# Kernel optimization log

Hardware: AMD Instinct MI355X
Metric: run time of the kernel (lower is better)

## Reference

```python
import jax, jax.numpy as jnp
import numpy as np

N = 102400          # total nodes (256 graphs x 400 nodes)
E = 3276800         # edges (avg degree 32)
B = 256             # num graphs
NODE_DIM, MRI_DIM, COG_DIM, CLIN_DIM, GEN_DIM, NUM_CLASSES = 128, 256, 64, 32, 512, 3
EPS = 1e-5

def _lin(k, i, o):
    kw, kb = jax.random.split(k)
    s = 1.0 / np.sqrt(i)
    return (jax.random.uniform(kw, (i, o), jnp.float32, -s, s),
            jax.random.uniform(kb, (o,), jnp.float32, -s, s))

def setup_inputs() -> dict:
    key = jax.random.key(0)
    ks = jax.random.split(key, 20)
    inp = {}
    inp['x'] = jax.random.normal(ks[0], (N, NODE_DIM), jnp.float32)
    inp['edge_index'] = jax.random.randint(ks[1], (2, E), 0, N)
    inp['batch'] = jnp.repeat(jnp.arange(B, dtype=jnp.int32), N // B)
    inp['mri'] = jax.random.normal(ks[2], (B, MRI_DIM), jnp.float32)
    inp['cog'] = jax.random.normal(ks[3], (B, COG_DIM), jnp.float32)
    inp['clin'] = jax.random.normal(ks[4], (B, CLIN_DIM), jnp.float32)
    inp['gen'] = jax.random.normal(ks[5], (B, GEN_DIM), jnp.float32)
    inp['W1'], inp['b1'] = _lin(ks[6], NODE_DIM, 64)
    inp['W2'], inp['b2'] = _lin(ks[7], 64, 32)
    inp['W3'], inp['b3'] = _lin(ks[8], 32, 16)
    inp['bn1_g'] = jnp.ones((64,), jnp.float32); inp['bn1_b'] = jnp.zeros((64,), jnp.float32)
    inp['bn2_g'] = jnp.ones((32,), jnp.float32); inp['bn2_b'] = jnp.zeros((32,), jnp.float32)
    inp['mriW'], inp['mrib'] = _lin(ks[9], MRI_DIM, 16)
    inp['cogW'], inp['cogb'] = _lin(ks[10], COG_DIM, 16)
    inp['clinW'], inp['clinb'] = _lin(ks[11], CLIN_DIM, 16)
    inp['genW'], inp['genb'] = _lin(ks[12], GEN_DIM, 16)
    inp['c1W'], inp['c1b'] = _lin(ks[13], 96, 64)  # 32 (pooled) + 64 (multimodal)
    inp['cbn1_g'] = jnp.ones((64,), jnp.float32); inp['cbn1_b'] = jnp.zeros((64,), jnp.float32)
    inp['c2W'], inp['c2b'] = _lin(ks[14], 64, 32)
    inp['cbn2_g'] = jnp.ones((32,), jnp.float32); inp['cbn2_b'] = jnp.zeros((32,), jnp.float32)
    inp['c3W'], inp['c3b'] = _lin(ks[15], 32, NUM_CLASSES)
    return inp

def _bn(h, g, b):
    # BatchNorm1d in training mode: biased batch stats
    m = h.mean(0)
    v = jnp.mean((h - m) ** 2, 0)
    return (h - m) * jax.lax.rsqrt(v + EPS) * g + b

def _gcn(h, W, bias, s, d, norm):
    # GCNConv: linear -> symmetric-normalized scatter-add aggregation (self-loops in s/d)
    h = h @ W
    agg = jnp.zeros_like(h).at[d].add(h[s] * norm[:, None])
    return agg + bias

def reference(x, edge_index, batch, mri, cog, clin, gen,
              W1, b1, W2, b2, W3, b3, bn1_g, bn1_b, bn2_g, bn2_b,
              mriW, mrib, cogW, cogb, clinW, clinb, genW, genb,
              c1W, c1b, cbn1_g, cbn1_b, c2W, c2b, cbn2_g, cbn2_b, c3W, c3b):
    n = x.shape[0]
    loop = jnp.arange(n)
    s = jnp.concatenate([edge_index[0], loop])
    d = jnp.concatenate([edge_index[1], loop])
    deg = jnp.zeros((n,), x.dtype).at[d].add(1.0)
    dinv = jax.lax.rsqrt(deg)  # deg >= 1 due to self-loops
    norm = dinv[s] * dinv[d]

    x1 = jax.nn.relu(_bn(_gcn(x, W1, b1, s, d, norm), bn1_g, bn1_b))
    x2 = jax.nn.relu(_bn(_gcn(x1, W2, b2, s, d, norm), bn2_g, bn2_b))
    gf = jax.nn.relu(_gcn(x2, W3, b3, s, d, norm))  # [N,16]

    cnt = jax.ops.segment_sum(jnp.ones((n,), x.dtype), batch, num_segments=B)
    g_mean = jax.ops.segment_sum(gf, batch, num_segments=B) / cnt[:, None]
    g_max = jax.ops.segment_max(gf, batch, num_segments=B)
    g_emb = jnp.concatenate([g_mean, g_max], axis=1)  # [B,32]

    mm = jnp.concatenate([
        jax.nn.relu(mri @ mriW + mrib),
        jax.nn.relu(cog @ cogW + cogb),
        jax.nn.relu(clin @ clinW + clinb),
        jax.nn.relu(gen @ genW + genb)], axis=1)  # [B,64]

    h = jnp.concatenate([g_emb, mm], axis=1)  # [B,96]
    h = jax.nn.relu(_bn(h @ c1W + c1b, cbn1_g, cbn1_b))  # dropout = identity (eval)
    h = jax.nn.relu(_bn(h @ c2W + c2b, cbn2_g, cbn2_b))
    out = h @ c3W + c3b
    return jax.nn.log_softmax(out, axis=1)
```

## Files before the change

kernel.cpp:

```cpp
#include <hip/hip_runtime.h>
#include <hip/hip_bf16.h>

#define TPB 256
#define BSHIFT 9
#define BNODES 512
#define CH 4096

typedef unsigned long long u64;
typedef __attribute__((ext_vector_type(8))) short short8;
typedef __attribute__((ext_vector_type(4))) float f32x4;

__device__ inline unsigned short f2bf(float f) {
    unsigned u = __float_as_uint(f);
    return (unsigned short)((u + 0x7FFF + ((u >> 16) & 1)) >> 16);
}
__device__ inline float bf2f(short s) {
    return __uint_as_float(((unsigned)(unsigned short)s) << 16);
}


__global__ void k_bhist(const int* __restrict__ dstp, int* __restrict__ bcnt, int E, int nbuk) {
    __shared__ int h[256];
    int tid = threadIdx.x;
    h[tid] = 0;
    __syncthreads();
    int e0 = blockIdx.x * CH;
    int e1 = min(e0 + CH, E);
    for (int e = e0 + tid; e < e1; e += TPB) atomicAdd(&h[dstp[e] >> BSHIFT], 1);
    __syncthreads();
    if (tid < nbuk && h[tid]) atomicAdd(&bcnt[tid], h[tid]);
}

__global__ void k_bscan(const int* __restrict__ bcnt, int* __restrict__ bbase,
                        int* __restrict__ gcur, int nbuk, int E) {
    __shared__ int s[256];
    int tid = threadIdx.x;
    int v = (tid < nbuk) ? bcnt[tid] : 0;
    s[tid] = v;
    __syncthreads();
    for (int o = 1; o < 256; o <<= 1) {
        int t = (tid >= o) ? s[tid - o] : 0;
        __syncthreads();
        s[tid] += t;
        __syncthreads();
    }
    if (tid < nbuk) { int e = s[tid] - v; bbase[tid] = e; gcur[tid] = e; }
    if (tid == 0) bbase[nbuk] = E;
}

__global__ void k_partition(const int* __restrict__ ei, int* __restrict__ gcur,
                            u64* __restrict__ part, int E, int nbuk) {
    __shared__ int h[256], baseg[256], scn[256], cur[256];
    __shared__ u64 stage[CH];
    int tid = threadIdx.x;
    h[tid] = 0;
    __syncthreads();
    int e0 = blockIdx.x * CH;
    int ecnt = min(CH, E - e0);
    const int* srcp = ei;
    const int* dstp = ei + E;
    for (int i = tid; i < ecnt; i += TPB) atomicAdd(&h[dstp[e0 + i] >> BSHIFT], 1);
    __syncthreads();
    int v = h[tid];
    if (tid < nbuk && v) baseg[tid] = atomicAdd(&gcur[tid], v);
    scn[tid] = v;
    __syncthreads();
    for (int o = 1; o < 256; o <<= 1) {
        int t = (tid >= o) ? scn[tid - o] : 0;
        __syncthreads();
        scn[tid] += t;
        __syncthreads();
    }
    int excl = scn[tid] - v;
    __syncthreads();
    scn[tid] = excl; cur[tid] = excl;
    __syncthreads();
    for (int i = tid; i < ecnt; i += TPB) {
        int s = srcp[e0 + i], d = dstp[e0 + i];
        int bk = d >> BSHIFT;
        int p = atomicAdd(&cur[bk], 1);
        stage[p] = ((u64)(unsigned)d << 32) | (unsigned)s;
    }
    __syncthreads();
    for (int i = tid; i < ecnt; i += TPB) {
        u64 vv = stage[i];
        int bk = (int)(vv >> 32) >> BSHIFT;
        part[baseg[bk] + (i - scn[bk])] = vv;
    }
}

__global__ void k_bucket_csr(const u64* __restrict__ part, const int* __restrict__ bbase,
                             float* __restrict__ dinv, int* __restrict__ offsets,
                             int* __restrict__ csr, int N, int nbuk) {
    __shared__ int cnt[BNODES];
    __shared__ int ps[256];
    __shared__ int off_s[BNODES];
    int b = blockIdx.x, tid = threadIdx.x;
    int n0 = b << BSHIFT;
    int nn = min(BNODES, N - n0);
    int j0 = bbase[b], j1 = bbase[b + 1];
    for (int i = tid; i < BNODES; i += TPB) cnt[i] = 0;
    __syncthreads();
    for (int j = j0 + tid; j < j1; j += TPB) {
        int dst = (int)(part[j] >> 32);
        atomicAdd(&cnt[dst - n0], 1);
    }
    __syncthreads();
    int a0 = cnt[2 * tid], a1 = cnt[2 * tid + 1];
    ps[tid] = a0 + a1;
    __syncthreads();
    for (int o = 1; o < 256; o <<= 1) {
        int t = (tid >= o) ? ps[tid - o] : 0;
        __syncthreads();
        ps[tid] += t;
        __syncthreads();
    }
    int excl = ps[tid] - (a0 + a1);
    off_s[2 * tid] = excl;
    off_s[2 * tid + 1] = excl + a0;
    __syncthreads();
    for (int i = tid; i < nn; i += TPB) {
        dinv[n0 + i] = rsqrtf((float)(cnt[i] + 1));
        offsets[n0 + i] = j0 + off_s[i];
    }
    if (b == nbuk - 1 && tid == 0) offsets[N] = j1;
    __syncthreads();
    for (int i = tid; i < BNODES; i += TPB) cnt[i] = j0 + off_s[i];
    __syncthreads();
    for (int j = j0 + tid; j < j1; j += TPB) {
        u64 vv = part[j];
        int dst = (int)(vv >> 32);
        int src = (int)(vv & 0xffffffffu);
        int pos = atomicAdd(&cnt[dst - n0], 1);
        csr[pos] = src;
    }
}


template<int K, bool BN, bool BF16IN>
__global__ void k_packA(const void* __restrict__ inv, const float* __restrict__ scale,
                        const float* __restrict__ shift, unsigned short* __restrict__ out) {
    constexpr int KB = K / 32;
    int g = blockIdx.x * TPB + threadIdx.x;
    int lane = g & 63, tile = g >> 6;
    int rowblk = tile / KB, kblk = tile - rowblk * KB;
    int row = rowblk * 16 + (lane & 15);
    int k0 = kblk * 32 + (lane >> 4) * 8;
    float vs[8];
    if (BF16IN) {
        const __hip_bfloat16* in = (const __hip_bfloat16*)inv;
        short8 sv = *reinterpret_cast<const short8*>(in + (size_t)row * K + k0);
        #pragma unroll
        for (int u = 0; u < 8; ++u) vs[u] = bf2f(sv[u]);
    } else {
        const float* in = (const float*)inv;
        const float4* p = reinterpret_cast<const float4*>(in + (size_t)row * K + k0);
        float4 v0 = p[0], v1 = p[1];
        vs[0] = v0.x; vs[1] = v0.y; vs[2] = v0.z; vs[3] = v0.w;
        vs[4] = v1.x; vs[5] = v1.y; vs[6] = v1.z; vs[7] = v1.w;
    }
    short8 rr;
    #pragma unroll
    for (int u = 0; u < 8; ++u) {
        float v = vs[u];
        if (BN) v = fmaxf(v * scale[k0 + u] + shift[k0 + u], 0.f);
        rr[u] = (short)f2bf(v);
    }
    *reinterpret_cast<short8*>(out + (size_t)g * 8) = rr;
}

__global__ void k_packW(const float* __restrict__ W1, const float* __restrict__ W2,
                        const float* __restrict__ W3, unsigned short* __restrict__ out) {
    int b = blockIdx.x, lane = threadIdx.x;
    const float* W; int KB, C; size_t off; int idx;
    if (b < 16)      { W = W1; KB = 4; C = 64; off = 0;     idx = b; }
    else if (b < 20) { W = W2; KB = 2; C = 32; off = 8192;  idx = b - 16; }
    else             { W = W3; KB = 1; C = 16; off = 10240; idx = b - 20; }
    int nblk = idx / KB, kblk = idx - nblk * KB;
    int col = nblk * 16 + (lane & 15);
    int k0 = kblk * 32 + (lane >> 4) * 8;
    short8 rr;
    #pragma unroll
    for (int j = 0; j < 8; ++j) rr[j] = (short)f2bf(W[(size_t)(k0 + j) * C + col]);
    *reinterpret_cast<short8*>(out + off + ((size_t)idx * 64 + lane) * 8) = rr;
}

template<int K, int C, int SW>
__global__ void k_mfma_gemm(const unsigned short* __restrict__ A,
                            const unsigned short* __restrict__ Wp,
                            const float* __restrict__ dinv,
                            __hip_bfloat16* __restrict__ hh, size_t slice) {
    constexpr int KB = K / 32, NB = C / 16;
    int lane = threadIdx.x & 63, w = threadIdx.x >> 6;
    int rowblk = blockIdx.x * 4 + w;
    const short8* Af = reinterpret_cast<const short8*>(A);
    const short8* Bf = reinterpret_cast<const short8*>(Wp);
    short8 b[NB][KB];
    #pragma unroll
    for (int nb = 0; nb < NB; ++nb)
        #pragma unroll
        for (int kb = 0; kb < KB; ++kb)
            b[nb][kb] = Bf[(nb * KB + kb) * 64 + lane];
    f32x4 z = {0.f, 0.f, 0.f, 0.f};
    f32x4 acc[NB];
    #pragma unroll
    for (int nb = 0; nb < NB; ++nb) acc[nb] = z;
    #pragma unroll
    for (int kb = 0; kb < KB; ++kb) {
        short8 a = Af[((size_t)rowblk * KB + kb) * 64 + lane];
        #pragma unroll
        for (int nb = 0; nb < NB; ++nb)
            acc[nb] = __builtin_amdgcn_mfma_f32_16x16x32_bf16(a, b[nb][kb], acc[nb], 0, 0, 0);
    }
    int colb = lane & 15;
    int node0 = rowblk * 16 + (lane >> 4) * 4;
    float dv[4];
    #pragma unroll
    for (int j = 0; j < 4; ++j) dv[j] = dinv[node0 + j];
    #pragma unroll
    for (int nb = 0; nb < NB; ++nb) {
        int c = nb * 16 + colb;
        size_t base = (size_t)(c / SW) * slice + (c % SW);
        #pragma unroll
        for (int j = 0; j < 4; ++j)
            hh[base + (size_t)(node0 + j) * SW] = __float2bfloat16(acc[nb][j] * dv[j]);
    }
}

template<int CT, bool RELU, bool STATS>
__global__ void k_gather_row32(const __hip_bfloat16* __restrict__ hhp,
                               const int* __restrict__ offs, const int* __restrict__ csr,
                               const float* __restrict__ dinv, const float* __restrict__ bias,
                               __hip_bfloat16* __restrict__ outp, float* __restrict__ pstat,
                               int n) {
    __shared__ float lred[16 * 528];
    __shared__ float sred[2 * 544];
    int tid = threadIdx.x;
    int g = tid >> 4, l = tid & 15;
    int node = blockIdx.x * 16 + g;
    int j0 = offs[node], j1 = offs[node + 1];
    float facc[32];
    #pragma unroll
    for (int u = 0; u < 32; ++u) facc[u] = 0.f;
    if (l == 15) {
        const short8* sr = reinterpret_cast<const short8*>(hhp + (size_t)node * 32);
        short8 r0 = sr[0], r1 = sr[1], r2 = sr[2], r3 = sr[3];
        #pragma unroll
        for (int u = 0; u < 8; ++u) {
            facc[u] += bf2f(r0[u]);      facc[8 + u]  += bf2f(r1[u]);
            facc[16 + u] += bf2f(r2[u]); facc[24 + u] += bf2f(r3[u]);
        }
    }
    int j = j0 + l;
    for (; j + 16 < j1; j += 32) {
        int s0 = __builtin_nontemporal_load(&csr[j]);
        int s1 = __builtin_nontemporal_load(&csr[j + 16]);
        const short8* ra = reinterpret_cast<const short8*>(hhp + (size_t)s0 * 32);
        const short8* rb = reinterpret_cast<const short8*>(hhp + (size_t)s1 * 32);
        short8 a0 = ra[0], a1 = ra[1], a2 = ra[2], a3 = ra[3];
        short8 b0 = rb[0], b1 = rb[1], b2 = rb[2], b3 = rb[3];
        #pragma unroll
        for (int u = 0; u < 8; ++u) {
            facc[u]      += bf2f(a0[u]) + bf2f(b0[u]);
            facc[8 + u]  += bf2f(a1[u]) + bf2f(b1[u]);
            facc[16 + u] += bf2f(a2[u]) + bf2f(b2[u]);
            facc[24 + u] += bf2f(a3[u]) + bf2f(b3[u]);
        }
    }
    if (j < j1) {
        int s = __builtin_nontemporal_load(&csr[j]);
        const short8* rr = reinterpret_cast<const short8*>(hhp + (size_t)s * 32);
        short8 r0 = rr[0], r1 = rr[1], r2 = rr[2], r3 = rr[3];
        #pragma unroll
        for (int u = 0; u < 8; ++u) {
            facc[u] += bf2f(r0[u]);      facc[8 + u]  += bf2f(r1[u]);
            facc[16 + u] += bf2f(r2[u]); facc[24 + u] += bf2f(r3[u]);
        }
    }
    int wbase = g * 528 + l * 33;
    #pragma unroll
    for (int u = 0; u < 32; ++u) lred[wbase + u] = facc[u];
    __syncthreads();
    int rbase = g * 528 + l;
    float alo = 0.f, ahi = 0.f;
    #pragma unroll
    for (int k = 0; k < 16; ++k) {
        alo += lred[rbase + k * 33];
        ahi += lred[rbase + k * 33 + 16];
    }
    float dv = dinv[node];
    float vlo = dv * alo + bias[l];
    float vhi = dv * ahi + bias[l + 16];
    if (RELU) { vlo = fmaxf(vlo, 0.f); vhi = fmaxf(vhi, 0.f); }
    outp[(size_t)node * CT + l]      = __float2bfloat16(vlo);
    outp[(size_t)node * CT + l + 16] = __float2bfloat16(vhi);
    if (STATS) {
        sred[l * 17 + g]          = vlo;
        sred[(l + 16) * 17 + g]   = vhi;
        sred[544 + l * 17 + g]        = vlo * vlo;
        sred[544 + (l + 16) * 17 + g] = vhi * vhi;
        __syncthreads();
        if (tid < 64) {
            int which = tid >> 5, c = tid & 31;
            const float* base = sred + which * 544 + c * 17;
            float a = 0.f;
            #pragma unroll
            for (int k = 0; k < 16; ++k) a += base[k];
            pstat[(size_t)blockIdx.x * 64 + which * 32 + c] = a;
        }
    }
}

template<int CT, bool RELU>
__global__ void k_gather_row(const __hip_bfloat16* __restrict__ hhp,
                             const int* __restrict__ offs, const int* __restrict__ csr,
                             const float* __restrict__ dinv, const float* __restrict__ bias,
                             __hip_bfloat16* __restrict__ outp, int n) {
    __shared__ float lred[16 * 272];
    int tid = threadIdx.x;
    int g = tid >> 4, l = tid & 15;
    int node = blockIdx.x * 16 + g;
    int j0 = offs[node], j1 = offs[node + 1];
    float facc[16];
    #pragma unroll
    for (int u = 0; u < 16; ++u) facc[u] = 0.f;
    if (l == 15) {
        const short8* sr = reinterpret_cast<const short8*>(hhp + (size_t)node * 16);
        short8 r0 = sr[0], r1 = sr[1];
        #pragma unroll
        for (int u = 0; u < 8; ++u) { facc[u] += bf2f(r0[u]); facc[8 + u] += bf2f(r1[u]); }
    }
    int j = j0 + l;
    for (; j + 16 < j1; j += 32) {
        int s0 = __builtin_nontemporal_load(&csr[j]);
        int s1 = __builtin_nontemporal_load(&csr[j + 16]);
        const short8* ra = reinterpret_cast<const short8*>(hhp + (size_t)s0 * 16);
        const short8* rb = reinterpret_cast<const short8*>(hhp + (size_t)s1 * 16);
        short8 a0 = ra[0], a1 = ra[1], b0 = rb[0], b1 = rb[1];
        #pragma unroll
        for (int u = 0; u < 8; ++u) {
            facc[u]     += bf2f(a0[u]) + bf2f(b0[u]);
            facc[8 + u] += bf2f(a1[u]) + bf2f(b1[u]);
        }
    }
    if (j < j1) {
        int s = __builtin_nontemporal_load(&csr[j]);
        const short8* rr = reinterpret_cast<const short8*>(hhp + (size_t)s * 16);
        short8 r0 = rr[0], r1 = rr[1];
        #pragma unroll
        for (int u = 0; u < 8; ++u) { facc[u] += bf2f(r0[u]); facc[8 + u] += bf2f(r1[u]); }
    }
    int wbase = g * 272 + l * 17;
    #pragma unroll
    for (int u = 0; u < 16; ++u) lred[wbase + u] = facc[u];
    __syncthreads();
    int rbase = g * 272 + l;
    float acc = 0.f;
    #pragma unroll
    for (int k = 0; k < 16; ++k) acc += lred[rbase + k * 17];
    float v = dinv[node] * acc + bias[l];
    if (RELU) v = fmaxf(v, 0.f);
    outp[(size_t)node * CT + l] = __float2bfloat16(v);
}

__global__ void k_bnred(const float* __restrict__ pstat, float* __restrict__ bred, int G) {
    __shared__ float ss[256];
    int tid = threadIdx.x;
    int p = blockIdx.x >> 6, c = blockIdx.x & 63;
    int rows_per = (G + 63) >> 6;
    int r0 = c * rows_per, r1 = min(r0 + rows_per, G);
    const float* base = pstat + (size_t)p * G * 64;
    float acc = 0.f;
    for (int i = r0 * 64 + tid; i < r1 * 64; i += 256) acc += base[i];
    ss[tid] = acc;
    __syncthreads();
    #pragma unroll
    for (int o = 128; o >= 64; o >>= 1) {
        if (tid < o) ss[tid] += ss[tid + o];
        __syncthreads();
    }
    if (tid < 64) bred[(size_t)blockIdx.x * 64 + tid] = ss[tid];
}

__global__ void k_bnstat2(const float* __restrict__ bred, const float* __restrict__ g,
                          const float* __restrict__ b, float* __restrict__ scale,
                          float* __restrict__ shift, float invN) {
    __shared__ float ss[256];
    int tid = threadIdx.x, p = blockIdx.x;
    const float* base = bred + (size_t)p * 64 * 64;
    float acc = 0.f;
    for (int i = tid; i < 64 * 64; i += 256) acc += base[i];
    ss[tid] = acc;
    __syncthreads();
    #pragma unroll
    for (int o = 128; o >= 64; o >>= 1) {
        if (tid < o) ss[tid] += ss[tid + o];
        __syncthreads();
    }
    if (tid < 32) {
        int ch = p * 32 + tid;
        float m = ss[tid] * invN;
        float var = ss[32 + tid] * invN - m * m;
        float sc = g[ch] * rsqrtf(var + 1e-5f);
        scale[ch] = sc;
        shift[ch] = b[ch] - m * sc;
    }
}

__global__ void k_graphhead(const __hip_bfloat16* __restrict__ gf, int nper,
                            const float* __restrict__ mri, const float* __restrict__ cog,
                            const float* __restrict__ clin, const float* __restrict__ gen,
                            const float* __restrict__ mriW, const float* __restrict__ mrib,
                            const float* __restrict__ cogW, const float* __restrict__ cogb,
                            const float* __restrict__ clinW, const float* __restrict__ clinb,
                            const float* __restrict__ genW, const float* __restrict__ genb,
                            const float* __restrict__ c1W, const float* __restrict__ c1b,
                            float* __restrict__ t1) {
    __shared__ float ssum[TPB], smax[TPB];
    __shared__ float hb[96];
    int b = blockIdx.x, tid = threadIdx.x;
    {
        int c = tid & 15, r0 = tid >> 4;
        const __hip_bfloat16* base = gf + (size_t)b * nper * 16;
        float s = 0.f, m = -1e30f;
        for (int r = r0; r < nper; r += 16) {
            float v = __bfloat162float(base[r * 16 + c]);
            s += v; m = fmaxf(m, v);
        }
        ssum[tid] = s; smax[tid] = m; __syncthreads();
        for (int off = 128; off >= 16; off >>= 1) {
            if (tid < off) { ssum[tid] += ssum[tid + off]; smax[tid] = fmaxf(smax[tid], smax[tid + off]); }
            __syncthreads();
        }
        if (tid < 16) { hb[tid] = ssum[tid] / (float)nper; hb[16 + tid] = smax[tid]; }
    }
    {
        int w = tid >> 6, lane = tid & 63;
        int c = lane & 15, part = lane >> 4;
        const float* in; const float* W; const float* bias; int K;
        if (w == 0)      { in = mri  + b * 256; W = mriW;  bias = mrib;  K = 256; }
        else if (w == 1) { in = cog  + b * 64;  W = cogW;  bias = cogb;  K = 64;  }
        else if (w == 2) { in = clin + b * 32;  W = clinW; bias = clinb; K = 32;  }
        else             { in = gen  + b * 512; W = genW;  bias = genb;  K = 512; }
        int kq = K >> 2, k0 = part * kq;
        float acc = 0.f;
        for (int k = k0; k < k0 + kq; k += 4) {
            float4 iv = *reinterpret_cast<const float4*>(in + k);
            acc += iv.x * W[k * 16 + c] + iv.y * W[(k + 1) * 16 + c]
                 + iv.z * W[(k + 2) * 16 + c] + iv.w * W[(k + 3) * 16 + c];
        }
        acc += __shfl_xor(acc, 16);
        acc += __shfl_xor(acc, 32);
        if (part == 0) hb[32 + w * 16 + c] = fmaxf(acc + bias[c], 0.f);
    }
    __syncthreads();
    if (tid < 64) {
        float acc = c1b[tid];
        #pragma unroll
        for (int k = 0; k < 96; ++k) acc += hb[k] * c1W[k * 64 + tid];
        t1[b * 64 + tid] = acc;
    }
}

__global__ __launch_bounds__(1024) void k_headtail(
        float* __restrict__ t1g,
        const float* __restrict__ cbn1_g, const float* __restrict__ cbn1_b,
        const float* __restrict__ c2W, const float* __restrict__ c2b,
        const float* __restrict__ cbn2_g, const float* __restrict__ cbn2_b,
        const float* __restrict__ c3W, const float* __restrict__ c3b,
        float* __restrict__ out) {
    __shared__ float red[1024];
    __shared__ float t2s[256 * 32];
    __shared__ float sc1[64], sh1[64], sc2[32], sh2[32];
    int tid = threadIdx.x;
    const float invB = 1.0f / 256.0f;

    float psum = 0.f, psq = 0.f;
    for (int i = tid; i < 16384; i += 1024) {
        float v = t1g[i]; psum += v; psq += v * v;
    }
    red[tid] = psum; __syncthreads();
    for (int o = 512; o >= 64; o >>= 1) { if (tid < o) red[tid] += red[tid + o]; __syncthreads(); }
    if (tid < 64) sc1[tid] = red[tid];
    __syncthreads();
    red[tid] = psq; __syncthreads();
    for (int o = 512; o >= 64; o >>= 1) { if (tid < o) red[tid] += red[tid + o]; __syncthreads(); }
    if (tid < 64) {
        float m = sc1[tid] * invB;
        float var = red[tid] * invB - m * m;
        float s = cbn1_g[tid] * rsqrtf(var + 1e-5f);
        sc1[tid] = s; sh1[tid] = cbn1_b[tid] - m * s;
    }
    __syncthreads();
    for (int i = tid; i < 16384; i += 1024) {
        int k = i & 63;
        t1g[i] = fmaxf(t1g[i] * sc1[k] + sh1[k], 0.f);
    }
    __syncthreads();
    int j2 = tid & 31, g2 = tid >> 5;
    float p2 = 0.f, q2 = 0.f;
    for (int b = g2 * 8; b < g2 * 8 + 8; ++b) {
        const float* tr = t1g + b * 64;
        float acc = c2b[j2];
        #pragma unroll
        for (int k = 0; k < 64; ++k) acc += tr[k] * c2W[k * 32 + j2];
        t2s[b * 32 + j2] = acc; p2 += acc; q2 += acc * acc;
    }
    red[tid] = p2; __syncthreads();
    for (int o = 512; o >= 32; o >>= 1) { if (tid < o) red[tid] += red[tid + o]; __syncthreads(); }
    if (tid < 32) sc2[tid] = red[tid];
    __syncthreads();
    red[tid] = q2; __syncthreads();
    for (int o = 512; o >= 32; o >>= 1) { if (tid < o) red[tid] += red[tid + o]; __syncthreads(); }
    if (tid < 32) {
        float m = sc2[tid] * invB;
        float var = red[tid] * invB - m * m;
        float s = cbn2_g[tid] * rsqrtf(var + 1e-5f);
        sc2[tid] = s; sh2[tid] = cbn2_b[tid] - m * s;
    }
    __syncthreads();
    if (tid < 256) {
        const float* tr = t2s + tid * 32;
        float o0 = c3b[0], o1 = c3b[1], o2 = c3b[2];
        #pragma unroll
        for (int k = 0; k < 32; ++k) {
            float v = fmaxf(tr[k] * sc2[k] + sh2[k], 0.f);
            o0 += v * c3W[k * 3 + 0];
            o1 += v * c3W[k * 3 + 1];
            o2 += v * c3W[k * 3 + 2];
        }
        float m = fmaxf(fmaxf(o0, o1), o2);
        float lse = m + logf(expf(o0 - m) + expf(o1 - m) + expf(o2 - m));
        out[tid * 3 + 0] = o0 - lse;
        out[tid * 3 + 1] = o1 - lse;
        out[tid * 3 + 2] = o2 - lse;
    }
}


extern "C" void kernel_launch(void* const* d_in, const int* in_sizes, int n_in,
                              void* d_out, int out_size, void* d_ws, size_t ws_size,
                              hipStream_t stream) {
    const float* x    = (const float*)d_in[0];
    const int*   ei   = (const int*)d_in[1];
    const float* mri  = (const float*)d_in[3];
    const float* cog  = (const float*)d_in[4];
    const float* clin = (const float*)d_in[5];
    const float* gen  = (const float*)d_in[6];
    const float* W1 = (const float*)d_in[7];  const float* b1 = (const float*)d_in[8];
    const float* W2 = (const float*)d_in[9];  const float* b2 = (const float*)d_in[10];
    const float* W3 = (const float*)d_in[11]; const float* b3 = (const float*)d_in[12];
    const float* bn1_g = (const float*)d_in[13]; const float* bn1_b = (const float*)d_in[14];
    const float* bn2_g = (const float*)d_in[15]; const float* bn2_b = (const float*)d_in[16];
    const float* mriW = (const float*)d_in[17]; const float* mrib = (const float*)d_in[18];
    const float* cogW = (const float*)d_in[19]; const float* cogb = (const float*)d_in[20];
    const float* clinW = (const float*)d_in[21]; const float* clinb = (const float*)d_in[22];
    const float* genW = (const float*)d_in[23]; const float* genb = (const float*)d_in[24];
    const float* c1W = (const float*)d_in[25]; const float* c1b = (const float*)d_in[26];
    const float* cbn1_g = (const float*)d_in[27]; const float* cbn1_b = (const float*)d_in[28];
    const float* c2W = (const float*)d_in[29]; const float* c2b = (const float*)d_in[30];
    const float* cbn2_g = (const float*)d_in[31]; const float* cbn2_b = (const float*)d_in[32];
    const float* c3W = (const float*)d_in[33]; const float* c3b = (const float*)d_in[34];
    float* out = (float*)d_out;

    const int N = in_sizes[0] / 128;
    const int E = in_sizes[1] / 2;
    const int B = in_sizes[6] / 512;
    const int nper = N / B;
    const int nbuk = (N + BNODES - 1) >> BSHIFT;
    const int npart = (E + CH - 1) / CH;
    const int rowblks = N / 16;
    const int G = N / 16;

    char* ws = (char*)d_ws;
    size_t off = 0;
    auto alloc = [&](size_t bytes) -> void* {
        void* p = ws + off;
        off += (bytes + 255) & ~(size_t)255;
        return p;
    };
    int*   bcnt    = (int*)alloc(256 * 4);
    int*   bbase   = (int*)alloc((size_t)(nbuk + 1) * 4);
    int*   gcur    = (int*)alloc((size_t)nbuk * 4);
    u64*   part    = (u64*)alloc((size_t)E * 8);
    __hip_bfloat16* agg = (__hip_bfloat16*)part;
    int*   offsets = (int*)alloc((size_t)(N + 1) * 4);
    int*   csr     = (int*)alloc((size_t)E * 4);
    float* dinv    = (float*)alloc((size_t)N * 4);
    __hip_bfloat16* hh = (__hip_bfloat16*)alloc((size_t)N * 64 * 2);
    unsigned short* xb = (unsigned short*)alloc((size_t)N * 128 * 2);
    unsigned short* Wpack = (unsigned short*)alloc(10752 * 2);
    float* pstat   = (float*)alloc((size_t)3 * G * 64 * 4);
    float* bred    = (float*)alloc((size_t)3 * 64 * 64 * 4);
    float* scale1  = (float*)alloc(64 * 4);
    float* shift1  = (float*)alloc(64 * 4);
    float* scale2  = (float*)alloc(32 * 4);
    float* shift2  = (float*)alloc(32 * 4);
    float* t1      = (float*)alloc((size_t)B * 64 * 4);
    (void)ws_size; (void)n_in; (void)out_size;

    hipMemsetAsync(bcnt, 0, 256 * 4, stream);

    k_bhist<<<npart, TPB, 0, stream>>>(ei + E, bcnt, E, nbuk);
    k_bscan<<<1, TPB, 0, stream>>>(bcnt, bbase, gcur, nbuk, E);
    k_partition<<<npart, TPB, 0, stream>>>(ei, gcur, part, E, nbuk);
    k_bucket_csr<<<nbuk, TPB, 0, stream>>>(part, bbase, dinv, offsets, csr, N, nbuk);
    k_packW<<<21, 64, 0, stream>>>(W1, W2, W3, Wpack);

    size_t slice32 = (size_t)N * 32;
    int gmm = rowblks / 4;

    k_packA<128, false, false><<<rowblks * 4 * 64 / TPB, TPB, 0, stream>>>(x, nullptr, nullptr, xb);
    k_mfma_gemm<128, 64, 32><<<gmm, TPB, 0, stream>>>(xb, Wpack, dinv, hh, slice32);
    for (int p = 0; p < 2; ++p)
        k_gather_row32<64, false, true><<<G, TPB, 0, stream>>>(
            hh + p * slice32, offsets, csr, dinv, b1 + p * 32,
            agg + p * 32, pstat + (size_t)p * G * 64, N);
    k_bnred<<<2 * 64, 256, 0, stream>>>(pstat, bred, G);
    k_bnstat2<<<2, 256, 0, stream>>>(bred, bn1_g, bn1_b, scale1, shift1, 1.0f / N);

    k_packA<64, true, true><<<rowblks * 2 * 64 / TPB, TPB, 0, stream>>>(agg, scale1, shift1, xb);
    k_mfma_gemm<64, 32, 32><<<gmm, TPB, 0, stream>>>(xb, Wpack + 8192, dinv, hh, slice32);
    k_gather_row32<32, false, true><<<G, TPB, 0, stream>>>(
        hh, offsets, csr, dinv, b2, agg, pstat + (size_t)2 * G * 64, N);
    k_bnred<<<64, 256, 0, stream>>>(pstat + (size_t)2 * G * 64, bred + 2 * 64 * 64, G);
    k_bnstat2<<<1, 256, 0, stream>>>(bred + 2 * 64 * 64, bn2_g, bn2_b, scale2, shift2, 1.0f / N);

    k_packA<32, true, true><<<rowblks * 1 * 64 / TPB, TPB, 0, stream>>>(agg, scale2, shift2, xb);
    k_mfma_gemm<32, 16, 16><<<gmm, TPB, 0, stream>>>(xb, Wpack + 10240, dinv, hh, (size_t)N * 16);
    k_gather_row<16, true><<<G, TPB, 0, stream>>>(hh, offsets, csr, dinv, b3, agg, N);

    k_graphhead<<<B, TPB, 0, stream>>>(agg, nper, mri, cog, clin, gen,
                                       mriW, mrib, cogW, cogb, clinW, clinb, genW, genb,
                                       c1W, c1b, t1);
    k_headtail<<<1, 1024, 0, stream>>>(t1, cbn1_g, cbn1_b, c2W, c2b,
                                       cbn2_g, cbn2_b, c3W, c3b, out);
}
```

Before: 382.1 us.

## Fuse packing kernels into early kernel, gather, and GEMM BN prologue

Merges the x-to-bf16 packing, edge bucket histogram and weight packing into one multi-role launch. The gather kernels now write their output directly in MFMA fragment layout through a shared-memory stage. The BatchNorm affine and ReLU move into the GEMM's A-operand load. Together these drop three separate packA launches and their intermediate buffer round trips, but add LDS staging and per-element BN work inside the GEMM loop.

```diff
diff --git a/kernel.cpp b/kernel.cpp
--- a/kernel.cpp
+++ b/kernel.cpp
@@ -18,18 +18,51 @@
     return __uint_as_float(((unsigned)(unsigned short)s) << 16);
 }
 
-
-__global__ void k_bhist(const int* __restrict__ dstp, int* __restrict__ bcnt, int E, int nbuk) {
+__global__ void k_early(const float* __restrict__ x, unsigned short* __restrict__ xb, int npA,
+                        const int* __restrict__ dstp, int* __restrict__ bcnt, int E,
+                        int nbuk, int npart,
+                        const float* __restrict__ W1, const float* __restrict__ W2,
+                        const float* __restrict__ W3, unsigned short* __restrict__ Wpack) {
     __shared__ int h[256];
-    int tid = threadIdx.x;
-    h[tid] = 0;
-    __syncthreads();
-    int e0 = blockIdx.x * CH;
-    int e1 = min(e0 + CH, E);
-    for (int e = e0 + tid; e < e1; e += TPB) atomicAdd(&h[dstp[e] >> BSHIFT], 1);
-    __syncthreads();
-    if (tid < nbuk && h[tid]) atomicAdd(&bcnt[tid], h[tid]);
-}
+    int blk = blockIdx.x, tid = threadIdx.x;
+    if (blk < npA) {
+        int g = blk * TPB + tid;
+        int lane = g & 63, tile = g >> 6;
+        int rowblk = tile >> 2, kblk = tile & 3;
+        int row = rowblk * 16 + (lane & 15);
+        int k0 = kblk * 32 + (lane >> 4) * 8;
+        const float4* p = reinterpret_cast<const float4*>(x + (size_t)row * 128 + k0);
+        float4 v0 = p[0], v1 = p[1];
+        float vs[8] = {v0.x, v0.y, v0.z, v0.w, v1.x, v1.y, v1.z, v1.w};
+        short8 rr;
+        #pragma unroll
+        for (int u = 0; u < 8; ++u) rr[u] = (short)f2bf(vs[u]);
+        *reinterpret_cast<short8*>(xb + (size_t)g * 8) = rr;
+    } else if (blk < npA + npart) {
+        int pb = blk - npA;
+        h[tid] = 0;
+        __syncthreads();
+        int e0 = pb * CH;
+        int e1 = min(e0 + CH, E);
+        for (int e = e0 + tid; e < e1; e += TPB) atomicAdd(&h[dstp[e] >> BSHIFT], 1);
+        __syncthreads();
+        if (tid < nbuk && h[tid]) atomicAdd(&bcnt[tid], h[tid]);
+    } else if (tid < 64) {
+        int b = blk - npA - npart;
+        const float* W; int KB, C; size_t off; int idx;
+        if (b < 16)      { W = W1; KB = 4; C = 64; off = 0;     idx = b; }
+        else if (b < 20) { W = W2; KB = 2; C = 32; off = 8192;  idx = b - 16; }
+        else             { W = W3; KB = 1; C = 16; off = 10240; idx = b - 20; }
+        int nblk = idx / KB, kblk = idx - nblk * KB;
+        int col = nblk * 16 + (tid & 15);
+        int k0 = kblk * 32 + (tid >> 4) * 8;
+        short8 rr;
+        #pragma unroll
+        for (int j = 0; j < 8; ++j) rr[j] = (short)f2bf(W[(size_t)(k0 + j) * C + col]);
+        *reinterpret_cast<short8*>(Wpack + off + ((size_t)idx * 64 + tid) * 8) = rr;
+    }
+}
+
 
 __global__ void k_bscan(const int* __restrict__ bcnt, int* __restrict__ bbase,
                         int* __restrict__ gcur, int nbuk, int E) {
@@ -136,58 +169,10 @@
     }
 }
 
-
-template<int K, bool BN, bool BF16IN>
-__global__ void k_packA(const void* __restrict__ inv, const float* __restrict__ scale,
-                        const float* __restrict__ shift, unsigned short* __restrict__ out) {
-    constexpr int KB = K / 32;
-    int g = blockIdx.x * TPB + threadIdx.x;
-    int lane = g & 63, tile = g >> 6;
-    int rowblk = tile / KB, kblk = tile - rowblk * KB;
-    int row = rowblk * 16 + (lane & 15);
-    int k0 = kblk * 32 + (lane >> 4) * 8;
-    float vs[8];
-    if (BF16IN) {
-        const __hip_bfloat16* in = (const __hip_bfloat16*)inv;
-        short8 sv = *reinterpret_cast<const short8*>(in + (size_t)row * K + k0);
-        #pragma unroll
-        for (int u = 0; u < 8; ++u) vs[u] = bf2f(sv[u]);
-    } else {
-        const float* in = (const float*)inv;
-        const float4* p = reinterpret_cast<const float4*>(in + (size_t)row * K + k0);
-        float4 v0 = p[0], v1 = p[1];
-        vs[0] = v0.x; vs[1] = v0.y; vs[2] = v0.z; vs[3] = v0.w;
-        vs[4] = v1.x; vs[5] = v1.y; vs[6] = v1.z; vs[7] = v1.w;
-    }
-    short8 rr;
-    #pragma unroll
-    for (int u = 0; u < 8; ++u) {
-        float v = vs[u];
-        if (BN) v = fmaxf(v * scale[k0 + u] + shift[k0 + u], 0.f);
-        rr[u] = (short)f2bf(v);
-    }
-    *reinterpret_cast<short8*>(out + (size_t)g * 8) = rr;
-}
-
-__global__ void k_packW(const float* __restrict__ W1, const float* __restrict__ W2,
-                        const float* __restrict__ W3, unsigned short* __restrict__ out) {
-    int b = blockIdx.x, lane = threadIdx.x;
-    const float* W; int KB, C; size_t off; int idx;
-    if (b < 16)      { W = W1; KB = 4; C = 64; off = 0;     idx = b; }
-    else if (b < 20) { W = W2; KB = 2; C = 32; off = 8192;  idx = b - 16; }
-    else             { W = W3; KB = 1; C = 16; off = 10240; idx = b - 20; }
-    int nblk = idx / KB, kblk = idx - nblk * KB;
-    int col = nblk * 16 + (lane & 15);
-    int k0 = kblk * 32 + (lane >> 4) * 8;
-    short8 rr;
-    #pragma unroll
-    for (int j = 0; j < 8; ++j) rr[j] = (short)f2bf(W[(size_t)(k0 + j) * C + col]);
-    *reinterpret_cast<short8*>(out + off + ((size_t)idx * 64 + lane) * 8) = rr;
-}
-
-template<int K, int C, int SW>
+template<int K, int C, int SW, bool BN>
 __global__ void k_mfma_gemm(const unsigned short* __restrict__ A,
                             const unsigned short* __restrict__ Wp,
+                            const float* __restrict__ scale, const float* __restrict__ shift,
                             const float* __restrict__ dinv,
                             __hip_bfloat16* __restrict__ hh, size_t slice) {
     constexpr int KB = K / 32, NB = C / 16;
@@ -208,6 +193,15 @@
     #pragma unroll
     for (int kb = 0; kb < KB; ++kb) {
         short8 a = Af[((size_t)rowblk * KB + kb) * 64 + lane];
+        if (BN) {
+            int k0 = kb * 32 + (lane >> 4) * 8;
+            #pragma unroll
+            for (int u = 0; u < 8; ++u) {
+                float v = bf2f(a[u]);
+                v = fmaxf(v * scale[k0 + u] + shift[k0 + u], 0.f);
+                a[u] = (short)f2bf(v);
+            }
+        }
         #pragma unroll
         for (int nb = 0; nb < NB; ++nb)
             acc[nb] = __builtin_amdgcn_mfma_f32_16x16x32_bf16(a, b[nb][kb], acc[nb], 0, 0, 0);
@@ -227,14 +221,15 @@
     }
 }
 
-template<int CT, bool RELU, bool STATS>
-__global__ void k_gather_row32(const __hip_bfloat16* __restrict__ hhp,
-                               const int* __restrict__ offs, const int* __restrict__ csr,
-                               const float* __restrict__ dinv, const float* __restrict__ bias,
-                               __hip_bfloat16* __restrict__ outp, float* __restrict__ pstat,
-                               int n) {
+template<bool STATS>
+__global__ void k_gather_frag32(const __hip_bfloat16* __restrict__ hhp,
+                                const int* __restrict__ offs, const int* __restrict__ csr,
+                                const float* __restrict__ dinv, const float* __restrict__ bias,
+                                unsigned short* __restrict__ frag, int KBN, int kblk,
+                                float* __restrict__ pstat, int n) {
     __shared__ float lred[16 * 528];
     __shared__ float sred[2 * 544];
+    __shared__ __align__(16) unsigned short fragstage[512];
     int tid = threadIdx.x;
     int g = tid >> 4, l = tid & 15;
     int node = blockIdx.x * 16 + g;
@@ -291,16 +286,19 @@
     float dv = dinv[node];
     float vlo = dv * alo + bias[l];
     float vhi = dv * ahi + bias[l + 16];
-    if (RELU) { vlo = fmaxf(vlo, 0.f); vhi = fmaxf(vhi, 0.f); }
-    outp[(size_t)node * CT + l]      = __float2bfloat16(vlo);
-    outp[(size_t)node * CT + l + 16] = __float2bfloat16(vhi);
+    fragstage[((((l >> 3) * 16 + g) << 3) | (l & 7))]       = f2bf(vlo);
+    fragstage[((((2 + (l >> 3)) * 16 + g) << 3) | (l & 7))] = f2bf(vhi);
     if (STATS) {
-        sred[l * 17 + g]          = vlo;
-        sred[(l + 16) * 17 + g]   = vhi;
+        sred[l * 17 + g]              = vlo;
+        sred[(l + 16) * 17 + g]       = vhi;
         sred[544 + l * 17 + g]        = vlo * vlo;
         sred[544 + (l + 16) * 17 + g] = vhi * vhi;
-        __syncthreads();
-        if (tid < 64) {
+    }
+    __syncthreads();
+    if (tid < 64) {
+        *reinterpret_cast<short8*>(frag + ((size_t)(blockIdx.x * KBN + kblk) * 64 + tid) * 8)
+            = *reinterpret_cast<const short8*>(&fragstage[(size_t)tid * 8]);
+        if (STATS) {
             int which = tid >> 5, c = tid & 31;
             const float* base = sred + which * 544 + c * 17;
             float a = 0.f;
@@ -571,6 +569,7 @@
     const int npart = (E + CH - 1) / CH;
     const int rowblks = N / 16;
     const int G = N / 16;
+    const int npA = rowblks;
 
     char* ws = (char*)d_ws;
     size_t off = 0;
@@ -601,33 +600,33 @@
 
     hipMemsetAsync(bcnt, 0, 256 * 4, stream);
 
-    k_bhist<<<npart, TPB, 0, stream>>>(ei + E, bcnt, E, nbuk);
+    k_early<<<npA + npart + 21, TPB, 0, stream>>>(x, xb, npA, ei + E, bcnt, E, nbuk, npart,
+                                                  W1, W2, W3, Wpack);
     k_bscan<<<1, TPB, 0, stream>>>(bcnt, bbase, gcur, nbuk, E);
     k_partition<<<npart, TPB, 0, stream>>>(ei, gcur, part, E, nbuk);
     k_bucket_csr<<<nbuk, TPB, 0, stream>>>(part, bbase, dinv, offsets, csr, N, nbuk);
-    k_packW<<<21, 64, 0, stream>>>(W1, W2, W3, Wpack);
 
     size_t slice32 = (size_t)N * 32;
     int gmm = rowblks / 4;
 
-    k_packA<128, false, false><<<rowblks * 4 * 64 / TPB, TPB, 0, stream>>>(x, nullptr, nullptr, xb);
-    k_mfma_gemm<128, 64, 32><<<gmm, TPB, 0, stream>>>(xb, Wpack, dinv, hh, slice32);
+    k_mfma_gemm<128, 64, 32, false><<<gmm, TPB, 0, stream>>>(xb, Wpack, nullptr, nullptr,
+                                                             dinv, hh, slice32);
     for (int p = 0; p < 2; ++p)
-        k_gather_row32<64, false, true><<<G, TPB, 0, stream>>>(
+        k_gather_frag32<true><<<G, TPB, 0, stream>>>(
             hh + p * slice32, offsets, csr, dinv, b1 + p * 32,
-            agg + p * 32, pstat + (size_t)p * G * 64, N);
+            xb, 2, p, pstat + (size_t)p * G * 64, N);
     k_bnred<<<2 * 64, 256, 0, stream>>>(pstat, bred, G);
     k_bnstat2<<<2, 256, 0, stream>>>(bred, bn1_g, bn1_b, scale1, shift1, 1.0f / N);
 
-    k_packA<64, true, true><<<rowblks * 2 * 64 / TPB, TPB, 0, stream>>>(agg, scale1, shift1, xb);
-    k_mfma_gemm<64, 32, 32><<<gmm, TPB, 0, stream>>>(xb, Wpack + 8192, dinv, hh, slice32);
-    k_gather_row32<32, false, true><<<G, TPB, 0, stream>>>(
-        hh, offsets, csr, dinv, b2, agg, pstat + (size_t)2 * G * 64, N);
+    k_mfma_gemm<64, 32, 32, true><<<gmm, TPB, 0, stream>>>(xb, Wpack + 8192, scale1, shift1,
+                                                           dinv, hh, slice32);
+    k_gather_frag32<true><<<G, TPB, 0, stream>>>(
+        hh, offsets, csr, dinv, b2, xb, 1, 0, pstat + (size_t)2 * G * 64, N);
     k_bnred<<<64, 256, 0, stream>>>(pstat + (size_t)2 * G * 64, bred + 2 * 64 * 64, G);
     k_bnstat2<<<1, 256, 0, stream>>>(bred + 2 * 64 * 64, bn2_g, bn2_b, scale2, shift2, 1.0f / N);
 
-    k_packA<32, true, true><<<rowblks * 1 * 64 / TPB, TPB, 0, stream>>>(agg, scale2, shift2, xb);
-    k_mfma_gemm<32, 16, 16><<<gmm, TPB, 0, stream>>>(xb, Wpack + 10240, dinv, hh, (size_t)N * 16);
+    k_mfma_gemm<32, 16, 16, true><<<gmm, TPB, 0, stream>>>(xb, Wpack + 10240, scale2, shift2,
+                                                           dinv, hh, (size_t)N * 16);
     k_gather_row<16, true><<<G, TPB, 0, stream>>>(hh, offsets, csr, dinv, b3, agg, N);
 
     k_graphhead<<<B, TPB, 0, stream>>>(agg, nper, mri, cog, clin, gen,
```

Result: faster. 368.8 us (-3.5%).
